# Kernel tuning notes

Hardware: AMD Instinct MI355X
Metric: run time of the kernel (lower is better)

The kernel has to match this reference:

```python
import jax, jax.numpy as jnp
import numpy as np

C32 = 768      # channels at stride 32 (convnextv2)
E = 4          # num_experts


def setup_inputs() -> dict:
    key = jax.random.key(0)
    ks = jax.random.split(key, 12)
    s = 0.02
    inp = {
        "s4":  jax.random.normal(ks[0], (8, 96, 256, 256), jnp.float32),
        "s8":  jax.random.normal(ks[1], (8, 192, 128, 128), jnp.float32),
        "s16": jax.random.normal(ks[2], (8, 384, 64, 64), jnp.float32),
        "s32": jax.random.normal(ks[3], (8, C32, 32, 32), jnp.float32),
        # 2-layer gate: C -> C -> E
        "gate_w1": jax.random.normal(ks[4], (C32, C32), jnp.float32) * s,
        "gate_b1": jnp.zeros((C32,), jnp.float32),
        "gate_w2": jax.random.normal(ks[5], (C32, E), jnp.float32) * s,
        "gate_b2": jnp.zeros((E,), jnp.float32),
        # E stacked ProtoExpert MLPs: C -> C -> C
        "exp_w1": jax.random.normal(ks[6], (E, C32, C32), jnp.float32) * s,
        "exp_b1": jnp.zeros((E, C32), jnp.float32),
        "exp_w2": jax.random.normal(ks[7], (E, C32, C32), jnp.float32) * s,
        "exp_b2": jnp.zeros((E, C32), jnp.float32),
    }
    return inp


def _vision_moe(x_bchw, gate_w1, gate_b1, gate_w2, gate_b2, exp_w1, exp_b1, exp_w2, exp_b2):
    B, C, H, W = x_bchw.shape
    x = x_bchw.transpose(0, 2, 3, 1).reshape(-1, C)            # [N, C] tokens
    # 2-layer gate -> softmax -> top-1 routing
    logits = jax.nn.gelu(x @ gate_w1 + gate_b1) @ gate_w2 + gate_b2  # [N, E]
    probs = jax.nn.softmax(logits, axis=-1)
    top_idx = jnp.argmax(probs, axis=-1)                        # [N]
    gate_val = jnp.take_along_axis(probs, top_idx[:, None], axis=-1)  # [N, 1]
    # dense all-expert compute, then select routed expert (jit-friendly)
    h = jax.nn.gelu(jnp.einsum('nc,ecd->ned', x, exp_w1) + exp_b1)    # [N, E, C]
    y_all = jnp.einsum('ned,edf->nef', h, exp_w2) + exp_b2            # [N, E, C]
    onehot = jax.nn.one_hot(top_idx, probs.shape[-1], dtype=x.dtype)  # [N, E]
    y = jnp.einsum('nef,ne->nf', y_all, onehot) * gate_val            # [N, C]
    return y.reshape(B, H, W, C).transpose(0, 3, 1, 2)


def reference(s4, s8, s16, s32, gate_w1, gate_b1, gate_w2, gate_b2, exp_w1, exp_b1, exp_w2, exp_b2):
    out32 = _vision_moe(s32, gate_w1, gate_b1, gate_w2, gate_b2,
                        exp_w1, exp_b1, exp_w2, exp_b2) + s32
    return (s4, s8, s16, out32)
```

## Files before the change

### kernel.cpp

```cpp
#include <hip/hip_runtime.h>
#include <cstddef>

#define CCH 768
#define NTOK 8192

typedef __attribute__((ext_vector_type(8))) short short8v;
typedef __attribute__((ext_vector_type(4))) float f32x4;

#define CHUNK 262144u
#define OFF_YT   0u
#define OFF_HH   25165824u
#define OFF_W2T  37748736u
#define OFF_AUX  42467328u
#define TAILBYTES 42729472u
#define OFF_XH   42729472u
#define OFF_W1T  55312384u
#define OFF_GWH  60030976u
#define OFF_GWL  62390272u
#define OFF_XL   64749568u
#define OFF_G    77332480u
#define S8DST    201326592u
#define S16DST   301989888u
#define OUTDST   352321536u

__device__ __forceinline__ void gl16(const void* g, void* l) {
    __builtin_amdgcn_global_load_lds(
        (const __attribute__((address_space(1))) void*)g,
        (__attribute__((address_space(3))) void*)l, 16, 0, 0);
}

__device__ __forceinline__ void copy_chunk_raw(const char* src, char* dst) {
    const uint4* s = (const uint4*)src;
    uint4* d = (uint4*)dst;
    int t = threadIdx.x;
#pragma unroll 8
    for (int it = 0; it < 64; ++it) d[it * 256 + t] = s[it * 256 + t];
}

__device__ __forceinline__ float gelu_tanh(float x) {
    float u = 0.7978845608028654f * (x + 0.044715f * x * x * x);
    float e = __expf(2.0f * u);
    float t = 1.0f - 2.0f / (e + 1.0f);
    return 0.5f * x * (1.0f + t);
}

__device__ __forceinline__ short f2b(float f) {
    unsigned u = __float_as_uint(f);
    unsigned r = (u + 0x7FFFu + ((u >> 16) & 1u)) >> 16;
    return (short)r;
}

__global__ __launch_bounds__(256) void k_prep(const float* __restrict__ s32,
                                              const float* __restrict__ gw1,
                                              const float* __restrict__ ew1,
                                              const float* __restrict__ ew2,
                                              short* __restrict__ Xh,
                                              short* __restrict__ Xl,
                                              short* __restrict__ GWh,
                                              short* __restrict__ GWl,
                                              short* __restrict__ W1T,
                                              short* __restrict__ W2T,
                                              int* __restrict__ az) {
    int z = blockIdx.z;
    int tx = threadIdx.x, ty = threadIdx.y;
    if (z == 0 && blockIdx.x == 0 && blockIdx.y == 0 && ty == 0 && tx < 8)
        az[tx] = 0;
    __shared__ float tile[32][33];
    if (z < 8) {
        int c0 = blockIdx.y * 32, hw0 = blockIdx.x * 32;
        const float* s = s32 + (size_t)z * CCH * 1024;
#pragma unroll
        for (int i = 0; i < 4; ++i)
            tile[ty + 8 * i][tx] = s[(size_t)(c0 + ty + 8 * i) * 1024 + hw0 + tx];
        __syncthreads();
#pragma unroll
        for (int i = 0; i < 4; ++i) {
            int r = ty + 8 * i;
            int n = z * 1024 + hw0 + r;
            float v = tile[tx][r];
            short h = f2b(v);
            float vh = __uint_as_float(((unsigned)(unsigned short)h) << 16);
            Xh[(size_t)n * CCH + c0 + tx] = h;
            Xl[(size_t)n * CCH + c0 + tx] = f2b(v - vh);
        }
    } else {
        if (blockIdx.x >= 24) return;
        int w = z - 8;
        const float* src;
        short *d1, *d2 = nullptr;
        if (w == 0) { src = gw1; d1 = GWh; d2 = GWl; }
        else if (w <= 4) { src = ew1 + (size_t)(w - 1) * CCH * CCH; d1 = W1T + (size_t)(w - 1) * CCH * CCH; }
        else { src = ew2 + (size_t)(w - 5) * CCH * CCH; d1 = W2T + (size_t)(w - 5) * CCH * CCH; }
        int ci0 = blockIdx.x * 32, co0 = blockIdx.y * 32;
#pragma unroll
        for (int i = 0; i < 4; ++i)
            tile[ty + 8 * i][tx] = src[(size_t)(ci0 + ty + 8 * i) * CCH + co0 + tx];
        __syncthreads();
#pragma unroll
        for (int i = 0; i < 4; ++i) {
            int co = co0 + ty + 8 * i;
            float v = tile[tx][ty + 8 * i];
            short h = f2b(v);
            d1[(size_t)co * CCH + ci0 + tx] = h;
            if (d2) {
                float vh = __uint_as_float(((unsigned)(unsigned short)h) << 16);
                d2[(size_t)co * CCH + ci0 + tx] = f2b(v - vh);
            }
        }
    }
}

template <int MODE>
__global__ __launch_bounds__(256) void k_mfma(const short* __restrict__ Ahp,
                                              const short* __restrict__ Alp,
                                              const short* __restrict__ Bhp,
                                              const short* __restrict__ Blp,
                                              const float* __restrict__ bias,
                                              const int* __restrict__ perm,
                                              const int* __restrict__ counts,
                                              const float* __restrict__ gval,
                                              float* __restrict__ Gout,
                                              short* __restrict__ Hout,
                                              const char* __restrict__ csrc1,
                                              const char* __restrict__ csrc2,
                                              char* __restrict__ bb,
                                              int ngemm) {
    int bid = blockIdx.x;
    if (bid >= ngemm) {
        int i = bid - ngemm;
        if (MODE == 0) {
            if (i < 377) { size_t c = (size_t)(391 + i) * CHUNK; copy_chunk_raw(csrc1 + c, bb + c); }
            else { size_t o = (size_t)(i - 377) * CHUNK; copy_chunk_raw(csrc2 + o, bb + S8DST + o); }
        } else if (MODE == 1) {
            size_t c = (size_t)(247 + i) * CHUNK; copy_chunk_raw(csrc1 + c, bb + c);
        } else {
            if (i < 84) { size_t c = (size_t)(163 + i) * CHUNK; copy_chunk_raw(csrc1 + c, bb + c); }
            else { size_t o = (size_t)(i - 84) * CHUNK; copy_chunk_raw(csrc2 + o, bb + S16DST + o); }
        }
        return;
    }
    int mt = bid / 6;
    int c0 = (bid % 6) * 128;
    int e = 0, ts = mt, cnt = 1 << 30, ofs = 0, mrow0 = 0;
    if (MODE == 0) {
        mrow0 = mt * 128;
    } else {
        e = mt >> 6;
        ts = mt & 63;
        int n0 = counts[0], n1 = counts[1], n2 = counts[2], n3 = counts[3];
        cnt = (e == 0) ? n0 : (e == 1) ? n1 : (e == 2) ? n2 : n3;
        if (ts * 128 >= cnt) return;
        ofs = (e > 0 ? n0 : 0) + (e > 1 ? n1 : 0) + (e > 2 ? n2 : 0);
    }
    __shared__ __align__(16) short lds[16384];

    int t = threadIdx.x;
    int lane = t & 63, w = t >> 6;
    int wr = w >> 1, wc = w & 1;
    int lrow = lane & 15, lk8 = lane >> 4;

    const short* aS[4];
    const short* bS[4];
    const short* alS[2];
    const short* blS[2];
    short* aD[4];
    short* bD[4];
    short* alD[2];
    short* blD[2];

    if (MODE == 0) {
#pragma unroll
        for (int i = 0; i < 2; ++i) {
            int c = 2 * w + i;
            int row = c * 16 + lrow;
            int koff = lk8 * 8;
            aS[i]  = Ahp + (size_t)(mrow0 + row) * CCH + koff;
            alS[i] = Alp + (size_t)(mrow0 + row) * CCH + koff;
            bS[i]  = Bhp + (size_t)(c0 + row) * CCH + koff;
            blS[i] = Blp + (size_t)(c0 + row) * CCH + koff;
            aD[i]  = lds + c * 512;
            bD[i]  = lds + 4096 + c * 512;
            alD[i] = lds + 8192 + c * 512;
            blD[i] = lds + 12288 + c * 512;
        }
    } else {
        size_t eoff = (size_t)e * CCH * CCH;
#pragma unroll
        for (int i = 0; i < 4; ++i) {
            int c = 4 * w + i;
            int g = c >> 1, ph = c & 1;
            int row = g * 16 + lrow;
            int koff = ph * 32 + lk8 * 8;
            int pl = ts * 128 + row;
            int pc = pl < cnt ? pl : cnt - 1;
            int tokrow = (MODE == 1) ? perm[ofs + pc] : (ofs + pc);
            aS[i] = Ahp + (size_t)tokrow * CCH + koff;
            bS[i] = Bhp + eoff + (size_t)(c0 + row) * CCH + koff;
            aD[i] = lds + c * 512;
            bD[i] = lds + 8192 + c * 512;
        }
    }

    f32x4 acc[4][4] = {};
    if (MODE == 0) {
        for (int k0 = 0; k0 < CCH; k0 += 32) {
#pragma unroll
            for (int i = 0; i < 2; ++i) {
                gl16(aS[i] + k0, aD[i]);
                gl16(bS[i] + k0, bD[i]);
                gl16(alS[i] + k0, alD[i]);
                gl16(blS[i] + k0, blD[i]);
            }
            __syncthreads();
            short8v af[4], bf[4], xf[4];
#pragma unroll
            for (int m = 0; m < 4; ++m)
                af[m] = *(const short8v*)(lds + ((wr * 4 + m) * 64 + lane) * 8);
#pragma unroll
            for (int n = 0; n < 4; ++n)
                bf[n] = *(const short8v*)(lds + 4096 + ((wc * 4 + n) * 64 + lane) * 8);
#pragma unroll
            for (int m = 0; m < 4; ++m)
#pragma unroll
                for (int n = 0; n < 4; ++n)
                    acc[m][n] = __builtin_amdgcn_mfma_f32_16x16x32_bf16(af[m], bf[n], acc[m][n], 0, 0, 0);
#pragma unroll
            for (int n = 0; n < 4; ++n)
                xf[n] = *(const short8v*)(lds + 12288 + ((wc * 4 + n) * 64 + lane) * 8);
#pragma unroll
            for (int m = 0; m < 4; ++m)
#pragma unroll
                for (int n = 0; n < 4; ++n)
                    acc[m][n] = __builtin_amdgcn_mfma_f32_16x16x32_bf16(af[m], xf[n], acc[m][n], 0, 0, 0);
#pragma unroll
            for (int m = 0; m < 4; ++m)
                xf[m] = *(const short8v*)(lds + 8192 + ((wr * 4 + m) * 64 + lane) * 8);
#pragma unroll
            for (int m = 0; m < 4; ++m)
#pragma unroll
                for (int n = 0; n < 4; ++n)
                    acc[m][n] = __builtin_amdgcn_mfma_f32_16x16x32_bf16(xf[m], bf[n], acc[m][n], 0, 0, 0);
            __syncthreads();
        }
    } else {
        for (int k0 = 0; k0 < CCH; k0 += 64) {
#pragma unroll
            for (int i = 0; i < 4; ++i) {
                gl16(aS[i] + k0, aD[i]);
                gl16(bS[i] + k0, bD[i]);
            }
            __syncthreads();
#pragma unroll
            for (int kk = 0; kk < 2; ++kk) {
                short8v af[4], bf[4];
#pragma unroll
                for (int m = 0; m < 4; ++m)
                    af[m] = *(const short8v*)(lds + (((wr * 4 + m) * 2 + kk) * 64 + lane) * 8);
#pragma unroll
                for (int n = 0; n < 4; ++n)
                    bf[n] = *(const short8v*)(lds + 8192 + (((wc * 4 + n) * 2 + kk) * 64 + lane) * 8);
#pragma unroll
                for (int m = 0; m < 4; ++m)
#pragma unroll
                    for (int n = 0; n < 4; ++n)
                        acc[m][n] = __builtin_amdgcn_mfma_f32_16x16x32_bf16(af[m], bf[n], acc[m][n], 0, 0, 0);
            }
            __syncthreads();
        }
    }

    int cl = lane & 15, rh = (lane >> 4) * 4;
#pragma unroll
    for (int n = 0; n < 4; ++n) {
        int col = c0 + wc * 64 + n * 16 + cl;
        float bv = (MODE == 0) ? bias[col] : bias[e * CCH + col];
#pragma unroll
        for (int m = 0; m < 4; ++m) {
#pragma unroll
            for (int ri = 0; ri < 4; ++ri) {
                int rr = wr * 64 + m * 16 + rh + ri;
                float v = acc[m][n][ri] + bv;
                if (MODE == 0) {
                    Gout[(size_t)(mrow0 + rr) * CCH + col] = gelu_tanh(v);
                } else {
                    int p = ts * 128 + rr;
                    if (p < cnt) {
                        if (MODE == 1) {
                            Hout[(size_t)(ofs + p) * CCH + col] = f2b(gelu_tanh(v));
                        } else {
                            int nn = perm[ofs + p];
                            Gout[(size_t)nn * CCH + col] = v * gval[nn];
                        }
                    }
                }
            }
        }
    }
}

__global__ __launch_bounds__(256) void k_gate2(const float* __restrict__ G,
                                               const float* __restrict__ W2,
                                               const float* __restrict__ b2,
                                               int* __restrict__ idx,
                                               float* __restrict__ gval,
                                               int* __restrict__ counts) {
    int t = threadIdx.x;
    int lane = t & 63, wid = t >> 6;
    int n = blockIdx.x * 4 + wid;
    const float* gr = G + (size_t)n * CCH;
    float a0 = 0.f, a1 = 0.f, a2 = 0.f, a3 = 0.f;
#pragma unroll
    for (int i = 0; i < 12; ++i) {
        int c = lane + 64 * i;
        float g = gr[c];
        float4 w = *(const float4*)(W2 + c * 4);
        a0 = fmaf(g, w.x, a0);
        a1 = fmaf(g, w.y, a1);
        a2 = fmaf(g, w.z, a2);
        a3 = fmaf(g, w.w, a3);
    }
#pragma unroll
    for (int off = 32; off > 0; off >>= 1) {
        a0 += __shfl_xor(a0, off);
        a1 += __shfl_xor(a1, off);
        a2 += __shfl_xor(a2, off);
        a3 += __shfl_xor(a3, off);
    }
    if (lane == 0) {
        float l0 = a0 + b2[0], l1 = a1 + b2[1], l2 = a2 + b2[2], l3 = a3 + b2[3];
        int e = 0;
        float m = l0;
        if (l1 > m) { m = l1; e = 1; }
        if (l2 > m) { m = l2; e = 2; }
        if (l3 > m) { m = l3; e = 3; }
        float s = __expf(l0 - m) + __expf(l1 - m) + __expf(l2 - m) + __expf(l3 - m);
        idx[n] = e;
        gval[n] = 1.0f / s;
        atomicAdd(counts + e, 1);
    }
}

__global__ __launch_bounds__(256) void k_scatter(const int* __restrict__ idx,
                                                 const int* __restrict__ counts,
                                                 int* __restrict__ cursors,
                                                 int* __restrict__ perm) {
    int n = blockIdx.x * 256 + threadIdx.x;
    int e = idx[n];
    int run = 0;
#pragma unroll
    for (int ee = 0; ee < 4; ++ee) {
        int c = counts[ee];
        if (e == ee) {
            int pos = run + atomicAdd(cursors + ee, 1);
            perm[pos] = n;
        }
        run += c;
    }
}

__global__ __launch_bounds__(256) void k_untr(const float* __restrict__ Yt,
                                              const float* __restrict__ s32,
                                              float* __restrict__ out32) {
    __shared__ float tile[32][33];
    int b = blockIdx.z;
    int c0 = blockIdx.y * 32, hw0 = blockIdx.x * 32;
    int tx = threadIdx.x, ty = threadIdx.y;
#pragma unroll
    for (int i = 0; i < 4; ++i) {
        int hwl = ty + 8 * i;
        tile[hwl][tx] = Yt[(size_t)(b * 1024 + hw0 + hwl) * CCH + c0 + tx];
    }
    __syncthreads();
    const float* sp = s32 + (size_t)b * CCH * 1024;
    float* op = out32 + (size_t)b * CCH * 1024;
#pragma unroll
    for (int i = 0; i < 4; ++i) {
        size_t a = (size_t)(c0 + ty + 8 * i) * 1024 + hw0 + tx;
        op[a] = tile[tx][ty + 8 * i] + sp[a];
    }
}

extern "C" void kernel_launch(void* const* d_in, const int* in_sizes, int n_in,
                              void* d_out, int out_size, void* d_ws, size_t ws_size,
                              hipStream_t stream) {
    const float* s4  = (const float*)d_in[0];
    const float* s8  = (const float*)d_in[1];
    const float* s16 = (const float*)d_in[2];
    const float* s32 = (const float*)d_in[3];
    const float* gw1 = (const float*)d_in[4];
    const float* gb1 = (const float*)d_in[5];
    const float* gw2 = (const float*)d_in[6];
    const float* gb2 = (const float*)d_in[7];
    const float* ew1 = (const float*)d_in[8];
    const float* eb1 = (const float*)d_in[9];
    const float* ew2 = (const float*)d_in[10];
    const float* eb2 = (const float*)d_in[11];

    char* bb = (char*)d_out;
    float* Yt   = (float*)(bb + OFF_YT);
    short* Hh   = (short*)(bb + OFF_HH);
    short* W2T  = (short*)(bb + OFF_W2T);
    int* iaux   = (int*)(bb + OFF_AUX);
    int* idx     = iaux;
    int* perm    = iaux + 8192;
    int* counts  = iaux + 16384;
    int* cursors = iaux + 16388;
    float* gval  = (float*)(iaux + 16392);
    short* Xh   = (short*)(bb + OFF_XH);
    short* W1T  = (short*)(bb + OFF_W1T);
    short* GWh  = (short*)(bb + OFF_GWH);
    short* GWl  = (short*)(bb + OFF_GWL);
    short* Xl   = (short*)(bb + OFF_XL);
    float* G    = (float*)(bb + OFF_G);
    float* out32 = (float*)(bb + OUTDST);

    k_prep<<<dim3(32, 24, 17), dim3(32, 8), 0, stream>>>(s32, gw1, ew1, ew2, Xh, Xl,
                                                         GWh, GWl, W1T, W2T, counts);
    k_mfma<0><<<384 + 761, 256, 0, stream>>>(Xh, Xl, GWh, GWl, gb1, perm, counts,
                                             gval, G, Hh,
                                             (const char*)s4, (const char*)s8, bb, 384);
    k_gate2<<<2048, 256, 0, stream>>>(G, gw2, gb2, idx, gval, counts);
    k_scatter<<<32, 256, 0, stream>>>(idx, counts, cursors, perm);
    k_mfma<1><<<1536 + 144, 256, 0, stream>>>(Xh, Xl, W1T, GWl, eb1, perm, counts,
                                              gval, G, Hh,
                                              (const char*)s4, (const char*)s16, bb, 1536);
    k_mfma<2><<<1536 + 276, 256, 0, stream>>>(Hh, Xl, W2T, GWl, eb2, perm, counts,
                                              gval, Yt, Hh,
                                              (const char*)s4, (const char*)s16, bb, 1536);
    k_untr<<<dim3(32, 24, 8), dim3(32, 8), 0, stream>>>(Yt, s32, out32);
    hipMemcpyAsync(bb, s4, (size_t)TAILBYTES, hipMemcpyDeviceToDevice, stream);
}
```

Before: 431.6 us.

## Fuse gate second layer into gate GEMM epilogue, double-buffer LDS, move weight prep

```diff
diff --git a/kernel.cpp b/kernel.cpp
--- a/kernel.cpp
+++ b/kernel.cpp
@@ -2,26 +2,29 @@
 #include <cstddef>
 
 #define CCH 768
-#define NTOK 8192
+#define CHUNK 262144u
+
+#define OFF_YT    0u
+#define OFF_HH    25165824u
+#define OFF_W2T   37748736u
+#define OFF_IDX   42467328u
+#define OFF_PERM  42500096u
+#define OFF_CNT   42532864u
+#define OFF_CUR   42532880u
+#define OFF_GVAL  42532896u
+#define OFF_PART  42565664u
+#define TAILBYTES 44564480u
+#define OFF_XL    44564480u
+#define OFF_GWH   57147392u
+#define OFF_GWL   58327040u
+#define OFF_XH    59506688u
+#define OFF_W1T   72089600u
+#define S8DST     201326592u
+#define S16DST    301989888u
+#define OUTDST    352321536u
 
 typedef __attribute__((ext_vector_type(8))) short short8v;
 typedef __attribute__((ext_vector_type(4))) float f32x4;
-
-#define CHUNK 262144u
-#define OFF_YT   0u
-#define OFF_HH   25165824u
-#define OFF_W2T  37748736u
-#define OFF_AUX  42467328u
-#define TAILBYTES 42729472u
-#define OFF_XH   42729472u
-#define OFF_W1T  55312384u
-#define OFF_GWH  60030976u
-#define OFF_GWL  62390272u
-#define OFF_XL   64749568u
-#define OFF_G    77332480u
-#define S8DST    201326592u
-#define S16DST   301989888u
-#define OUTDST   352321536u
 
 __device__ __forceinline__ void gl16(const void* g, void* l) {
     __builtin_amdgcn_global_load_lds(
@@ -52,14 +55,10 @@
 
 __global__ __launch_bounds__(256) void k_prep(const float* __restrict__ s32,
                                               const float* __restrict__ gw1,
-                                              const float* __restrict__ ew1,
-                                              const float* __restrict__ ew2,
                                               short* __restrict__ Xh,
                                               short* __restrict__ Xl,
                                               short* __restrict__ GWh,
                                               short* __restrict__ GWl,
-                                              short* __restrict__ W1T,
-                                              short* __restrict__ W2T,
                                               int* __restrict__ az) {
     int z = blockIdx.z;
     int tx = threadIdx.x, ty = threadIdx.y;
@@ -85,27 +84,19 @@
         }
     } else {
         if (blockIdx.x >= 24) return;
-        int w = z - 8;
-        const float* src;
-        short *d1, *d2 = nullptr;
-        if (w == 0) { src = gw1; d1 = GWh; d2 = GWl; }
-        else if (w <= 4) { src = ew1 + (size_t)(w - 1) * CCH * CCH; d1 = W1T + (size_t)(w - 1) * CCH * CCH; }
-        else { src = ew2 + (size_t)(w - 5) * CCH * CCH; d1 = W2T + (size_t)(w - 5) * CCH * CCH; }
         int ci0 = blockIdx.x * 32, co0 = blockIdx.y * 32;
 #pragma unroll
         for (int i = 0; i < 4; ++i)
-            tile[ty + 8 * i][tx] = src[(size_t)(ci0 + ty + 8 * i) * CCH + co0 + tx];
+            tile[ty + 8 * i][tx] = gw1[(size_t)(ci0 + ty + 8 * i) * CCH + co0 + tx];
         __syncthreads();
 #pragma unroll
         for (int i = 0; i < 4; ++i) {
             int co = co0 + ty + 8 * i;
             float v = tile[tx][ty + 8 * i];
             short h = f2b(v);
-            d1[(size_t)co * CCH + ci0 + tx] = h;
-            if (d2) {
-                float vh = __uint_as_float(((unsigned)(unsigned short)h) << 16);
-                d2[(size_t)co * CCH + ci0 + tx] = f2b(v - vh);
-            }
+            GWh[(size_t)co * CCH + ci0 + tx] = h;
+            float vh = __uint_as_float(((unsigned)(unsigned short)h) << 16);
+            GWl[(size_t)co * CCH + ci0 + tx] = f2b(v - vh);
         }
     }
 }
@@ -116,31 +107,75 @@
                                               const short* __restrict__ Bhp,
                                               const short* __restrict__ Blp,
                                               const float* __restrict__ bias,
+                                              const float* __restrict__ gw2,
                                               const int* __restrict__ perm,
                                               const int* __restrict__ counts,
                                               const float* __restrict__ gval,
-                                              float* __restrict__ Gout,
+                                              float* __restrict__ Yt,
                                               short* __restrict__ Hout,
+                                              float* __restrict__ partial,
+                                              const float* __restrict__ ew1,
+                                              const float* __restrict__ ew2,
+                                              short* __restrict__ W1T,
+                                              short* __restrict__ W2T,
                                               const char* __restrict__ csrc1,
                                               const char* __restrict__ csrc2,
                                               char* __restrict__ bb,
                                               int ngemm) {
+    __shared__ __align__(16) short lds[32768];
     int bid = blockIdx.x;
+    int t = threadIdx.x;
     if (bid >= ngemm) {
         int i = bid - ngemm;
         if (MODE == 0) {
-            if (i < 377) { size_t c = (size_t)(391 + i) * CHUNK; copy_chunk_raw(csrc1 + c, bb + c); }
-            else { size_t o = (size_t)(i - 377) * CHUNK; copy_chunk_raw(csrc2 + o, bb + S8DST + o); }
+            if (i < 475) {
+                size_t c = (size_t)(293 + i) * CHUNK;
+                copy_chunk_raw(csrc1 + c, bb + c);
+            } else if (i < 859) {
+                size_t o = (size_t)(i - 475) * CHUNK;
+                copy_chunk_raw(csrc2 + o, bb + S8DST + o);
+            } else {
+                int j = i - 859;
+                int mat = j / 576, q = j % 576;
+                int ci0 = (q % 24) * 32, co0 = (q / 24) * 32;
+                const float* src = (mat < 4 ? ew1 : ew2) + (size_t)(mat & 3) * CCH * CCH;
+                short* dst = (mat < 4 ? W1T : W2T) + (size_t)(mat & 3) * CCH * CCH;
+                float* tile = (float*)lds;
+                int tx = t & 31, ty = t >> 5;
+#pragma unroll
+                for (int i4 = 0; i4 < 4; ++i4)
+                    tile[(ty + 8 * i4) * 33 + tx] =
+                        src[(size_t)(ci0 + ty + 8 * i4) * CCH + co0 + tx];
+                __syncthreads();
+#pragma unroll
+                for (int i4 = 0; i4 < 4; ++i4) {
+                    int co = co0 + ty + 8 * i4;
+                    dst[(size_t)co * CCH + ci0 + tx] = f2b(tile[tx * 33 + ty + 8 * i4]);
+                }
+            }
         } else if (MODE == 1) {
-            size_t c = (size_t)(247 + i) * CHUNK; copy_chunk_raw(csrc1 + c, bb + c);
+            if (i < 57) {
+                size_t c = (size_t)(170 + i) * CHUNK;
+                copy_chunk_raw(csrc1 + c, bb + c);
+            } else {
+                size_t o = (size_t)(i - 57) * CHUNK;
+                copy_chunk_raw(csrc2 + o, bb + S16DST + o);
+            }
         } else {
-            if (i < 84) { size_t c = (size_t)(163 + i) * CHUNK; copy_chunk_raw(csrc1 + c, bb + c); }
-            else { size_t o = (size_t)(i - 84) * CHUNK; copy_chunk_raw(csrc2 + o, bb + S16DST + o); }
+            if (i < 66) {
+                size_t c = (size_t)(227 + i) * CHUNK;
+                copy_chunk_raw(csrc1 + c, bb + c);
+            } else {
+                size_t o = (size_t)(96 + i - 66) * CHUNK;
+                copy_chunk_raw(csrc2 + (size_t)(i - 66) * CHUNK, bb + S16DST + o - (size_t)96 * CHUNK + (size_t)96 * CHUNK);
+            }
         }
         return;
     }
+
+    int cbk = bid % 6;
     int mt = bid / 6;
-    int c0 = (bid % 6) * 128;
+    int c0 = cbk * 128;
     int e = 0, ts = mt, cnt = 1 << 30, ofs = 0, mrow0 = 0;
     if (MODE == 0) {
         mrow0 = mt * 128;
@@ -152,9 +187,7 @@
         if (ts * 128 >= cnt) return;
         ofs = (e > 0 ? n0 : 0) + (e > 1 ? n1 : 0) + (e > 2 ? n2 : 0);
     }
-    __shared__ __align__(16) short lds[16384];
-
-    int t = threadIdx.x;
+
     int lane = t & 63, w = t >> 6;
     int wr = w >> 1, wc = w & 1;
     int lrow = lane & 15, lk8 = lane >> 4;
@@ -163,10 +196,7 @@
     const short* bS[4];
     const short* alS[2];
     const short* blS[2];
-    short* aD[4];
-    short* bD[4];
-    short* alD[2];
-    short* blD[2];
+    int dA[4];
 
     if (MODE == 0) {
 #pragma unroll
@@ -178,10 +208,7 @@
             alS[i] = Alp + (size_t)(mrow0 + row) * CCH + koff;
             bS[i]  = Bhp + (size_t)(c0 + row) * CCH + koff;
             blS[i] = Blp + (size_t)(c0 + row) * CCH + koff;
-            aD[i]  = lds + c * 512;
-            bD[i]  = lds + 4096 + c * 512;
-            alD[i] = lds + 8192 + c * 512;
-            blD[i] = lds + 12288 + c * 512;
+            dA[i] = c * 512;
         }
     } else {
         size_t eoff = (size_t)e * CCH * CCH;
@@ -196,29 +223,36 @@
             int tokrow = (MODE == 1) ? perm[ofs + pc] : (ofs + pc);
             aS[i] = Ahp + (size_t)tokrow * CCH + koff;
             bS[i] = Bhp + eoff + (size_t)(c0 + row) * CCH + koff;
-            aD[i] = lds + c * 512;
-            bD[i] = lds + 8192 + c * 512;
+            dA[i] = c * 512;
         }
     }
 
     f32x4 acc[4][4] = {};
+
     if (MODE == 0) {
-        for (int k0 = 0; k0 < CCH; k0 += 32) {
+        auto stage = [&](int b, int k0) {
+            short* L = lds + b * 16384;
 #pragma unroll
             for (int i = 0; i < 2; ++i) {
-                gl16(aS[i] + k0, aD[i]);
-                gl16(bS[i] + k0, bD[i]);
-                gl16(alS[i] + k0, alD[i]);
-                gl16(blS[i] + k0, blD[i]);
-            }
-            __syncthreads();
+                gl16(aS[i] + k0, L + dA[i]);
+                gl16(bS[i] + k0, L + 4096 + dA[i]);
+                gl16(alS[i] + k0, L + 8192 + dA[i]);
+                gl16(blS[i] + k0, L + 12288 + dA[i]);
+            }
+        };
+        stage(0, 0);
+        __syncthreads();
+        for (int tt = 0; tt < 24; ++tt) {
+            int cur = tt & 1;
+            if (tt < 23) stage(cur ^ 1, (tt + 1) * 32);
+            const short* L = lds + cur * 16384;
             short8v af[4], bf[4], xf[4];
 #pragma unroll
             for (int m = 0; m < 4; ++m)
-                af[m] = *(const short8v*)(lds + ((wr * 4 + m) * 64 + lane) * 8);
+                af[m] = *(const short8v*)(L + ((wr * 4 + m) * 64 + lane) * 8);
 #pragma unroll
             for (int n = 0; n < 4; ++n)
-                bf[n] = *(const short8v*)(lds + 4096 + ((wc * 4 + n) * 64 + lane) * 8);
+                bf[n] = *(const short8v*)(L + 4096 + ((wc * 4 + n) * 64 + lane) * 8);
 #pragma unroll
             for (int m = 0; m < 4; ++m)
 #pragma unroll
@@ -226,7 +260,7 @@
                     acc[m][n] = __builtin_amdgcn_mfma_f32_16x16x32_bf16(af[m], bf[n], acc[m][n], 0, 0, 0);
 #pragma unroll
             for (int n = 0; n < 4; ++n)
-                xf[n] = *(const short8v*)(lds + 12288 + ((wc * 4 + n) * 64 + lane) * 8);
+                xf[n] = *(const short8v*)(L + 12288 + ((wc * 4 + n) * 64 + lane) * 8);
 #pragma unroll
             for (int m = 0; m < 4; ++m)
 #pragma unroll
@@ -234,7 +268,7 @@
                     acc[m][n] = __builtin_amdgcn_mfma_f32_16x16x32_bf16(af[m], xf[n], acc[m][n], 0, 0, 0);
 #pragma unroll
             for (int m = 0; m < 4; ++m)
-                xf[m] = *(const short8v*)(lds + 8192 + ((wr * 4 + m) * 64 + lane) * 8);
+                xf[m] = *(const short8v*)(L + 8192 + ((wr * 4 + m) * 64 + lane) * 8);
 #pragma unroll
             for (int m = 0; m < 4; ++m)
 #pragma unroll
@@ -243,22 +277,29 @@
             __syncthreads();
         }
     } else {
-        for (int k0 = 0; k0 < CCH; k0 += 64) {
+        auto stage = [&](int b, int k0) {
+            short* L = lds + b * 16384;
 #pragma unroll
             for (int i = 0; i < 4; ++i) {
-                gl16(aS[i] + k0, aD[i]);
-                gl16(bS[i] + k0, bD[i]);
-            }
-            __syncthreads();
+                gl16(aS[i] + k0, L + dA[i]);
+                gl16(bS[i] + k0, L + 8192 + dA[i]);
+            }
+        };
+        stage(0, 0);
+        __syncthreads();
+        for (int tt = 0; tt < 12; ++tt) {
+            int cur = tt & 1;
+            if (tt < 11) stage(cur ^ 1, (tt + 1) * 64);
+            const short* L = lds + cur * 16384;
 #pragma unroll
             for (int kk = 0; kk < 2; ++kk) {
                 short8v af[4], bf[4];
 #pragma unroll
                 for (int m = 0; m < 4; ++m)
-                    af[m] = *(const short8v*)(lds + (((wr * 4 + m) * 2 + kk) * 64 + lane) * 8);
+                    af[m] = *(const short8v*)(L + (((wr * 4 + m) * 2 + kk) * 64 + lane) * 8);
 #pragma unroll
                 for (int n = 0; n < 4; ++n)
-                    bf[n] = *(const short8v*)(lds + 8192 + (((wc * 4 + n) * 2 + kk) * 64 + lane) * 8);
+                    bf[n] = *(const short8v*)(L + 8192 + (((wc * 4 + n) * 2 + kk) * 64 + lane) * 8);
 #pragma unroll
                 for (int m = 0; m < 4; ++m)
 #pragma unroll
@@ -270,26 +311,61 @@
     }
 
     int cl = lane & 15, rh = (lane >> 4) * 4;
-#pragma unroll
-    for (int n = 0; n < 4; ++n) {
-        int col = c0 + wc * 64 + n * 16 + cl;
-        float bv = (MODE == 0) ? bias[col] : bias[e * CCH + col];
+    if (MODE == 0) {
+        int cb2 = cbk * 2 + wc;
+        float bv[4];
+        float4 w2v[4];
+#pragma unroll
+        for (int n_ = 0; n_ < 4; ++n_) {
+            int col = c0 + wc * 64 + n_ * 16 + cl;
+            bv[n_] = bias[col];
+            w2v[n_] = *(const float4*)(gw2 + col * 4);
+        }
 #pragma unroll
         for (int m = 0; m < 4; ++m) {
 #pragma unroll
             for (int ri = 0; ri < 4; ++ri) {
-                int rr = wr * 64 + m * 16 + rh + ri;
-                float v = acc[m][n][ri] + bv;
-                if (MODE == 0) {
-                    Gout[(size_t)(mrow0 + rr) * CCH + col] = gelu_tanh(v);
-                } else {
-                    int p = ts * 128 + rr;
+                float s0 = 0.f, s1 = 0.f, s2 = 0.f, s3 = 0.f;
+#pragma unroll
+                for (int n_ = 0; n_ < 4; ++n_) {
+                    float g = gelu_tanh(acc[m][n_][ri] + bv[n_]);
+                    s0 = fmaf(g, w2v[n_].x, s0);
+                    s1 = fmaf(g, w2v[n_].y, s1);
+                    s2 = fmaf(g, w2v[n_].z, s2);
+                    s3 = fmaf(g, w2v[n_].w, s3);
+                }
+#pragma unroll
+                for (int off = 1; off < 16; off <<= 1) {
+                    s0 += __shfl_xor(s0, off);
+                    s1 += __shfl_xor(s1, off);
+                    s2 += __shfl_xor(s2, off);
+                    s3 += __shfl_xor(s3, off);
+                }
+                if (cl == 0) {
+                    int row = mrow0 + wr * 64 + m * 16 + rh + ri;
+                    float4 pv;
+                    pv.x = s0; pv.y = s1; pv.z = s2; pv.w = s3;
+                    *(float4*)(partial + (size_t)(cb2 * 8192 + row) * 4) = pv;
+                }
+            }
+        }
+    } else {
+#pragma unroll
+        for (int n = 0; n < 4; ++n) {
+            int col = c0 + wc * 64 + n * 16 + cl;
+            float bv = bias[e * CCH + col];
+#pragma unroll
+            for (int m = 0; m < 4; ++m) {
+#pragma unroll
+                for (int ri = 0; ri < 4; ++ri) {
+                    int p = ts * 128 + wr * 64 + m * 16 + rh + ri;
                     if (p < cnt) {
+                        float v = acc[m][n][ri] + bv;
                         if (MODE == 1) {
                             Hout[(size_t)(ofs + p) * CCH + col] = f2b(gelu_tanh(v));
                         } else {
                             int nn = perm[ofs + p];
-                            Gout[(size_t)nn * CCH + col] = v * gval[nn];
+                            Yt[(size_t)nn * CCH + col] = v * gval[nn];
                         }
                     }
                 }
@@ -298,46 +374,27 @@
     }
 }
 
-__global__ __launch_bounds__(256) void k_gate2(const float* __restrict__ G,
-                                               const float* __restrict__ W2,
+__global__ __launch_bounds__(256) void k_route(const float* __restrict__ partial,
                                                const float* __restrict__ b2,
                                                int* __restrict__ idx,
                                                float* __restrict__ gval,
                                                int* __restrict__ counts) {
-    int t = threadIdx.x;
-    int lane = t & 63, wid = t >> 6;
-    int n = blockIdx.x * 4 + wid;
-    const float* gr = G + (size_t)n * CCH;
-    float a0 = 0.f, a1 = 0.f, a2 = 0.f, a3 = 0.f;
-#pragma unroll
-    for (int i = 0; i < 12; ++i) {
-        int c = lane + 64 * i;
-        float g = gr[c];
-        float4 w = *(const float4*)(W2 + c * 4);
-        a0 = fmaf(g, w.x, a0);
-        a1 = fmaf(g, w.y, a1);
-        a2 = fmaf(g, w.z, a2);
-        a3 = fmaf(g, w.w, a3);
-    }
-#pragma unroll
-    for (int off = 32; off > 0; off >>= 1) {
-        a0 += __shfl_xor(a0, off);
-        a1 += __shfl_xor(a1, off);
-        a2 += __shfl_xor(a2, off);
-        a3 += __shfl_xor(a3, off);
-    }
-    if (lane == 0) {
-        float l0 = a0 + b2[0], l1 = a1 + b2[1], l2 = a2 + b2[2], l3 = a3 + b2[3];
-        int e = 0;
-        float m = l0;
-        if (l1 > m) { m = l1; e = 1; }
-        if (l2 > m) { m = l2; e = 2; }
-        if (l3 > m) { m = l3; e = 3; }
-        float s = __expf(l0 - m) + __expf(l1 - m) + __expf(l2 - m) + __expf(l3 - m);
-        idx[n] = e;
-        gval[n] = 1.0f / s;
-        atomicAdd(counts + e, 1);
-    }
+    int n = blockIdx.x * 256 + threadIdx.x;
+    float l0 = b2[0], l1 = b2[1], l2 = b2[2], l3 = b2[3];
+#pragma unroll
+    for (int p = 0; p < 12; ++p) {
+        float4 v = *(const float4*)(partial + ((size_t)p * 8192 + n) * 4);
+        l0 += v.x; l1 += v.y; l2 += v.z; l3 += v.w;
+    }
+    int e = 0;
+    float m = l0;
+    if (l1 > m) { m = l1; e = 1; }
+    if (l2 > m) { m = l2; e = 2; }
+    if (l3 > m) { m = l3; e = 3; }
+    float s = __expf(l0 - m) + __expf(l1 - m) + __expf(l2 - m) + __expf(l3 - m);
+    idx[n] = e;
+    gval[n] = 1.0f / s;
+    atomicAdd(counts + e, 1);
 }
 
 __global__ __launch_bounds__(256) void k_scatter(const int* __restrict__ idx,
@@ -397,36 +454,40 @@
     const float* eb2 = (const float*)d_in[11];
 
     char* bb = (char*)d_out;
-    float* Yt   = (float*)(bb + OFF_YT);
-    short* Hh   = (short*)(bb + OFF_HH);
-    short* W2T  = (short*)(bb + OFF_W2T);
-    int* iaux   = (int*)(bb + OFF_AUX);
-    int* idx     = iaux;
-    int* perm    = iaux + 8192;
-    int* counts  = iaux + 16384;
-    int* cursors = iaux + 16388;
-    float* gval  = (float*)(iaux + 16392);
-    short* Xh   = (short*)(bb + OFF_XH);
-    short* W1T  = (short*)(bb + OFF_W1T);
-    short* GWh  = (short*)(bb + OFF_GWH);
-    short* GWl  = (short*)(bb + OFF_GWL);
-    short* Xl   = (short*)(bb + OFF_XL);
-    float* G    = (float*)(bb + OFF_G);
-    float* out32 = (float*)(bb + OUTDST);
-
-    k_prep<<<dim3(32, 24, 17), dim3(32, 8), 0, stream>>>(s32, gw1, ew1, ew2, Xh, Xl,
-                                                         GWh, GWl, W1T, W2T, counts);
-    k_mfma<0><<<384 + 761, 256, 0, stream>>>(Xh, Xl, GWh, GWl, gb1, perm, counts,
-                                             gval, G, Hh,
-                                             (const char*)s4, (const char*)s8, bb, 384);
-    k_gate2<<<2048, 256, 0, stream>>>(G, gw2, gb2, idx, gval, counts);
+    float* Yt      = (float*)(bb + OFF_YT);
+    short* Hh      = (short*)(bb + OFF_HH);
+    short* W2T     = (short*)(bb + OFF_W2T);
+    int*   idx     = (int*)(bb + OFF_IDX);
+    int*   perm    = (int*)(bb + OFF_PERM);
+    int*   counts  = (int*)(bb + OFF_CNT);
+    int*   cursors = (int*)(bb + OFF_CUR);
+    float* gval    = (float*)(bb + OFF_GVAL);
+    float* partial = (float*)(bb + OFF_PART);
+    short* Xl      = (short*)(bb + OFF_XL);
+    short* GWh     = (short*)(bb + OFF_GWH);
+    short* GWl     = (short*)(bb + OFF_GWL);
+    short* Xh      = (short*)(bb + OFF_XH);
+    short* W1T     = (short*)(bb + OFF_W1T);
+    float* out32   = (float*)(bb + OUTDST);
+
+    k_prep<<<dim3(32, 24, 9), dim3(32, 8), 0, stream>>>(s32, gw1, Xh, Xl, GWh, GWl, counts);
+    k_mfma<0><<<384 + 859 + 4608, 256, 0, stream>>>(Xh, Xl, GWh, GWl, gb1, gw2,
+                                                    perm, counts, gval, Yt, Hh,
+                                                    partial, ew1, ew2, W1T, W2T,
+                                                    (const char*)s4, (const char*)s8,
+                                                    bb, 384);
+    k_route<<<32, 256, 0, stream>>>(partial, gb2, idx, gval, counts);
     k_scatter<<<32, 256, 0, stream>>>(idx, counts, cursors, perm);
-    k_mfma<1><<<1536 + 144, 256, 0, stream>>>(Xh, Xl, W1T, GWl, eb1, perm, counts,
-                                              gval, G, Hh,
-                                              (const char*)s4, (const char*)s16, bb, 1536);
-    k_mfma<2><<<1536 + 276, 256, 0, stream>>>(Hh, Xl, W2T, GWl, eb2, perm, counts,
-                                              gval, Yt, Hh,
-                                              (const char*)s4, (const char*)s16, bb, 1536);
+    k_mfma<1><<<1536 + 153, 256, 0, stream>>>(Xh, Xl, W1T, GWl, eb1, gw2,
+                                              perm, counts, gval, Yt, Hh,
+                                              partial, ew1, ew2, W1T, W2T,
+                                              (const char*)s4, (const char*)s16,
+                                              bb, 1536);
+    k_mfma<2><<<1536 + 162, 256, 0, stream>>>(Hh, Xl, W2T, GWl, eb2, gw2,
+                                              perm, counts, gval, Yt, Hh,
+                                              partial, ew1, ew2, W1T, W2T,
+                                              (const char*)s4, (const char*)(s16 + (size_t)96 * CHUNK / 4),
+                                              bb, 1536);
     k_untr<<<dim3(32, 24, 8), dim3(32, 8), 0, stream>>>(Yt, s32, out32);
     hipMemcpyAsync(bb, s4, (size_t)TAILBYTES, hipMemcpyDeviceToDevice, stream);
 }
```

After: 371.5 us. 13.9% less time.
